# Kernel tuning notes

Measured on AMD Instinct MI355X. Metric: run time of the kernel, lower is better.

Reference implementation:

```python
import jax, jax.numpy as jnp
import numpy as np

N_EMBD = 512
N_HEAD = 8
EPS = 1e-5


def setup_inputs() -> dict:
    key = jax.random.key(0)
    ks = jax.random.split(key, 8)
    C = N_EMBD
    s = lambda k, shape, fan: jax.random.normal(k, shape, jnp.float32) * (1.0 / np.sqrt(fan))
    return {
        "x": jax.random.normal(ks[0], (2, 4096, C), jnp.float32),
        "w_qkv": s(ks[1], (C, 3 * C), C), "b_qkv": jnp.zeros((3 * C,), jnp.float32),
        "w_attn_proj": s(ks[2], (C, C), C), "b_attn_proj": jnp.zeros((C,), jnp.float32),
        "w_fc": s(ks[3], (C, 4 * C), C), "b_fc": jnp.zeros((4 * C,), jnp.float32),
        "w_mlp_proj": s(ks[4], (4 * C, C), 4 * C), "b_mlp_proj": jnp.zeros((C,), jnp.float32),
        "ln1_g": jnp.ones((C,), jnp.float32), "ln1_b": jnp.zeros((C,), jnp.float32),
        "ln2_g": jnp.ones((C,), jnp.float32), "ln2_b": jnp.zeros((C,), jnp.float32),
    }


def _layernorm(x, g, b):
    mu = jnp.mean(x, axis=-1, keepdims=True)
    var = jnp.mean(jnp.square(x - mu), axis=-1, keepdims=True)
    return (x - mu) * jax.lax.rsqrt(var + EPS) * g + b


def _attention(x, w_qkv, b_qkv, w_proj, b_proj):
    B, T, C = x.shape
    hd = C // N_HEAD
    qkv = x @ w_qkv + b_qkv  # [B,T,3C]
    q, k, v = jnp.split(qkv, 3, axis=-1)
    q = q.reshape(B, T, N_HEAD, hd)
    k = k.reshape(B, T, N_HEAD, hd)
    v = v.reshape(B, T, N_HEAD, hd)
    # NOTE: faithful to source -- scale by sqrt(C) (n_embd), not sqrt(head_dim)
    scores = jnp.einsum('bthd,bshd->bhts', q, k) / jnp.sqrt(jnp.float32(C))
    mask = jnp.tril(jnp.ones((T, T), bool))
    scores = jnp.where(mask, scores, -jnp.inf)
    attn = jax.nn.softmax(scores, axis=-1)  # [B,H,T,T]
    y = jnp.einsum('bhts,bshd->bthd', attn, v).reshape(B, T, C)
    return y @ w_proj + b_proj


def _mlp(x, w_fc, b_fc, w_proj, b_proj):
    h = jax.nn.gelu(x @ w_fc + b_fc, approximate=True)
    return h @ w_proj + b_proj


def reference(x, w_qkv, b_qkv, w_attn_proj, b_attn_proj, w_fc, b_fc,
              w_mlp_proj, b_mlp_proj, ln1_g, ln1_b, ln2_g, ln2_b):
    x = x + _attention(_layernorm(x, ln1_g, ln1_b), w_qkv, b_qkv, w_attn_proj, b_attn_proj)
    x = x + _mlp(_layernorm(x, ln2_g, ln2_b), w_fc, b_fc, w_mlp_proj, b_mlp_proj)
    return x
```

## Files before the change

### kernel.cpp

```cpp
#include <hip/hip_runtime.h>
#include <hip/hip_bf16.h>
#include <math.h>

constexpr int B_ = 2;
constexpr int T_ = 4096;
constexpr int C_ = 512;
constexpr int H_ = 8;
constexpr int BT_ = B_ * T_;
constexpr float EPS_ = 1e-5f;

typedef __attribute__((ext_vector_type(8))) short bf16x8;
typedef __attribute__((ext_vector_type(4))) short short4v;
typedef __attribute__((ext_vector_type(8))) short short8v;
typedef __attribute__((ext_vector_type(4))) float f32x4;

__device__ __forceinline__ short f2bf(float f) {
    unsigned int u = __float_as_uint(f);
    unsigned int r = (u + 0x7fffu + ((u >> 16) & 1u)) >> 16;
    return (short)r;
}
__device__ __forceinline__ float bf2f(short s) {
    return __uint_as_float(((unsigned)(unsigned short)s) << 16);
}
__device__ __forceinline__ short f2bf_h(float f) {
    union { __hip_bfloat16 h; short s; } u;
    u.h = __float2bfloat16(f);
    return u.s;
}
__device__ __forceinline__ float exp2_f(float x) {
    float r;
    asm("v_exp_f32 %0, %1" : "=v"(r) : "v"(x));
    return r;
}

__device__ __forceinline__ float gelu_f(float v) {
    const float k0 = 0.7978845608028654f;
    const float k1 = 0.044715f;
    return 0.5f * v * (1.0f + tanhf(k0 * (v + k1 * v * v * v)));
}

__device__ __forceinline__ void gl_lds16(const short* gsrc, short* lds) {
    __builtin_amdgcn_global_load_lds(
        (const __attribute__((address_space(1))) void*)gsrc,
        (__attribute__((address_space(3))) void*)lds, 16, 0, 0);
}

__global__ __launch_bounds__(256) void transpose_w4(
    const float* __restrict__ W0, short* __restrict__ D0,
    const float* __restrict__ W1, short* __restrict__ D1,
    const float* __restrict__ W2, short* __restrict__ D2,
    const float* __restrict__ W3, short* __restrict__ D3) {
    __shared__ float tile[32][33];
    int bid = blockIdx.x;
    const float* W; short* D; int K, N, nx;
    if (bid < 768)       {             W = W0; D = D0; K = 512;  N = 1536; nx = 48; }
    else if (bid < 1024) { bid -= 768;  W = W1; D = D1; K = 512;  N = 512;  nx = 16; }
    else if (bid < 2048) { bid -= 1024; W = W2; D = D2; K = 512;  N = 2048; nx = 64; }
    else                 { bid -= 2048; W = W3; D = D3; K = 2048; N = 512;  nx = 16; }
    const int n0 = (bid % nx) * 32, k0 = (bid / nx) * 32;
    const int tx = threadIdx.x & 31, ty = threadIdx.x >> 5;
    #pragma unroll
    for (int j = 0; j < 4; j++)
        tile[ty + j * 8][tx] = W[(size_t)(k0 + ty + j * 8) * N + n0 + tx];
    __syncthreads();
    #pragma unroll
    for (int j = 0; j < 4; j++)
        D[(size_t)(n0 + ty + j * 8) * K + k0 + tx] = f2bf(tile[tx][ty + j * 8]);
}

__global__ __launch_bounds__(256) void ln_bf16(const float* __restrict__ x,
                                               const float* __restrict__ g,
                                               const float* __restrict__ b,
                                               short* __restrict__ out) {
    const int row = blockIdx.x * 4 + (threadIdx.x >> 6);
    const int lane = threadIdx.x & 63;
    const float* xr = x + (size_t)row * C_;

    float4 v0 = *(const float4*)(xr + lane * 8);
    float4 v1 = *(const float4*)(xr + lane * 8 + 4);

    float s  = v0.x + v0.y + v0.z + v0.w + v1.x + v1.y + v1.z + v1.w;
    float s2 = v0.x*v0.x + v0.y*v0.y + v0.z*v0.z + v0.w*v0.w
             + v1.x*v1.x + v1.y*v1.y + v1.z*v1.z + v1.w*v1.w;
    #pragma unroll
    for (int off = 32; off; off >>= 1) {
        s  += __shfl_down(s, off);
        s2 += __shfl_down(s2, off);
    }
    s  = __shfl(s, 0);
    s2 = __shfl(s2, 0);

    const float mu  = s * (1.0f / C_);
    const float var = s2 * (1.0f / C_) - mu * mu;
    const float rs  = rsqrtf(var + EPS_);

    float4 g0 = *(const float4*)(g + lane * 8);
    float4 g1 = *(const float4*)(g + lane * 8 + 4);
    float4 b0 = *(const float4*)(b + lane * 8);
    float4 b1 = *(const float4*)(b + lane * 8 + 4);

    short8v o;
    o[0] = f2bf((v0.x - mu) * rs * g0.x + b0.x);
    o[1] = f2bf((v0.y - mu) * rs * g0.y + b0.y);
    o[2] = f2bf((v0.z - mu) * rs * g0.z + b0.z);
    o[3] = f2bf((v0.w - mu) * rs * g0.w + b0.w);
    o[4] = f2bf((v1.x - mu) * rs * g1.x + b1.x);
    o[5] = f2bf((v1.y - mu) * rs * g1.y + b1.y);
    o[6] = f2bf((v1.z - mu) * rs * g1.z + b1.z);
    o[7] = f2bf((v1.w - mu) * rs * g1.w + b1.w);
    *(short8v*)(out + (size_t)row * C_ + lane * 8) = o;
}

template<int ACT, int OUTBF16, int HASRES, int VFUSE>
__global__ __launch_bounds__(256) void gemm_bf16(const short* __restrict__ A,
                                                 const short* __restrict__ Wt,
                                                 const float* __restrict__ bias,
                                                 const float* __restrict__ res,
                                                 void* __restrict__ outp,
                                                 int M, int N, int K,
                                                 int GX, int CY,
                                                 short* __restrict__ vtb) {
    __shared__ short As[64 * 128];
    __shared__ short Bs[128 * 128];

    const int bid = blockIdx.x;
    const int xcd = bid & 7, jb = bid >> 3;
    const int by = xcd * CY + jb / GX;
    const int bx = jb % GX;

    const int t = threadIdx.x;
    const int w = t >> 6;
    const int l = t & 63;
    const int c = l & 15;
    const int g = l >> 4;
    const int wr = w >> 1, wc = w & 1;
    const int m0 = by * 64, n0 = bx * 128;

    const int r16 = t >> 4;
    const int sch = ((t & 15) ^ (r16 & 7)) * 8;
    const short* Asrc = A  + (size_t)(m0 + r16) * K + sch;
    const short* Bsrc = Wt + (size_t)(n0 + r16) * K + sch;

    auto stage = [&](int kt) {
        #pragma unroll
        for (int i = 0; i < 4; i++)
            gl_lds16(Asrc + (size_t)(16 * i) * K + kt, &As[i * 2048 + w * 512]);
        #pragma unroll
        for (int i = 0; i < 8; i++)
            gl_lds16(Bsrc + (size_t)(16 * i) * K + kt, &Bs[i * 2048 + w * 512]);
    };

    f32x4 acc[2][4] = {};

    for (int kt = 0; kt < K; kt += 128) {
        stage(kt);
        __syncthreads();

        #pragma unroll
        for (int j = 0; j < 4; j++) {
            const int ckj = ((4 * j + g) ^ (c & 7)) * 8;
            bf16x8 af[2], bfr[4];
            #pragma unroll
            for (int mt = 0; mt < 2; mt++)
                af[mt] = *(const bf16x8*)&As[(wr * 32 + mt * 16 + c) * 128 + ckj];
            #pragma unroll
            for (int nt = 0; nt < 4; nt++)
                bfr[nt] = *(const bf16x8*)&Bs[(wc * 64 + nt * 16 + c) * 128 + ckj];
            #pragma unroll
            for (int mt = 0; mt < 2; mt++)
                #pragma unroll
                for (int nt = 0; nt < 4; nt++)
                    acc[mt][nt] = __builtin_amdgcn_mfma_f32_16x16x32_bf16(
                        af[mt], bfr[nt], acc[mt][nt], 0, 0, 0);
        }

        __syncthreads();
    }

    const int colb = n0 + wc * 64;
    float bias_v[4];
    #pragma unroll
    for (int nt = 0; nt < 4; nt++) bias_v[nt] = bias[colb + nt * 16 + c];

    if (VFUSE && n0 >= 1024) {
        const int bq   = m0 >> 12;
        const int trow = (m0 & 4095) + wr * 32;
        #pragma unroll
        for (int mt = 0; mt < 2; mt++) {
            const int tb = trow + 8 * g + 4 * mt;
            #pragma unroll
            for (int nt = 0; nt < 4; nt++) {
                const int vcol = colb + nt * 16 + c - 1024;
                const int hh = vcol >> 6, dd = vcol & 63;
                short4v pk;
                #pragma unroll
                for (int rr = 0; rr < 4; rr++)
                    pk[rr] = f2bf(acc[mt][nt][rr] + bias_v[nt]);
                *(short4v*)&vtb[((size_t)((bq * 8 + hh) * 64 + dd)) * T_ + tb] = pk;
            }
        }
        return;
    }

    float* out_f = (float*)outp;
    short* out_h = (short*)outp;

    #pragma unroll
    for (int mt = 0; mt < 2; mt++) {
        #pragma unroll
        for (int rr = 0; rr < 4; rr++) {
            const size_t row = (size_t)(m0 + wr * 32 + mt * 16 + 4 * g + rr);
            #pragma unroll
            for (int nt = 0; nt < 4; nt++) {
                const int col = colb + nt * 16 + c;
                float v = acc[mt][nt][rr] + bias_v[nt];
                if (ACT) v = gelu_f(v);
                if (HASRES) v += res[row * N + col];
                if (OUTBF16) out_h[row * N + col] = f2bf(v);
                else         out_f[row * N + col] = v;
            }
        }
    }
}

__global__ __launch_bounds__(256) void attn_mfma(const short* __restrict__ qkv,
                                                 const short* __restrict__ Vt,
                                                 short* __restrict__ y) {
    __shared__ union {
        struct { short K[2][64 * 64]; short V[2][64 * 64]; } s;
        float O[4][16][68];
    } sm;

    const int bid = blockIdx.x;
    const int xcd = bid & 7, jj = bid >> 3;
    const int lo = jj >> 6;
    const int qtr = jj & 63;
    const int qt = (qtr < 32) ? (63 - qtr) : (qtr - 32);
    const int g16 = xcd * 2 + lo;
    const int b = g16 >> 3, h = g16 & 7;

    const int tid = threadIdx.x, w = tid >> 6, lid = tid & 63;
    const int c = lid & 15, g = lid >> 4;
    const size_t base = (size_t)b * T_;
    const int bh = g16;

    const float qmul = 0.04419417382415922f * 1.4426950408889634f;

    bf16x8 qf0, qf1;
    {
        const short* qa = qkv + (base + qt * 64 + w * 16 + c) * 1536 + h * 64 + g * 8;
        bf16x8 a0 = *(const bf16x8*)qa;
        bf16x8 a1 = *(const bf16x8*)(qa + 32);
        #pragma unroll
        for (int i = 0; i < 8; i++) {
            qf0[i] = f2bf_h(bf2f(a0[i]) * qmul);
            qf1[i] = f2bf_h(bf2f(a1[i]) * qmul);
        }
    }

    const f32x4 kZero = {0.f, 0.f, 0.f, 0.f};
    bf16x8 kOnes;
    #pragma unroll
    for (int i = 0; i < 8; i++) kOnes[i] = (short)0x3F80;

    f32x4 ot[4] = {};
    f32x4 lacc = {0.f, 0.f, 0.f, 0.f};
    const int qg = qt * 64 + w * 16 + c;

    const int sr = tid >> 3;
    const int sc = ((tid & 7) ^ (sr & 7)) * 8;

    auto stage = [&](short* Kb, short* Vb, int st) {
        const short* ks = qkv + (base + st * 64 + sr) * 1536 + 512 + h * 64 + sc;
        const short* vs = Vt + ((size_t)(bh * 64 + sr)) * T_ + st * 64 + sc;
        gl_lds16(ks, Kb + w * 512);
        gl_lds16(ks + (size_t)32 * 1536, Kb + 2048 + w * 512);
        gl_lds16(vs, Vb + w * 512);
        gl_lds16(vs + (size_t)32 * T_, Vb + 2048 + w * 512);
    };

    const int rx = c & 7;
    const int ck0 = g ^ rx;
    const int ck1 = ck0 ^ 4;

    auto tile = [&](const short* Kb, const short* Vb, bool mask_diag) {
        f32x4 s[4];
        __builtin_amdgcn_s_setprio(1);
        #pragma unroll
        for (int mt = 0; mt < 4; mt++) {
            const short* krow = Kb + (mt * 16 + c) * 64;
            bf16x8 k0 = *(const bf16x8*)&krow[ck0 * 8];
            bf16x8 k1 = *(const bf16x8*)&krow[ck1 * 8];
            f32x4 z = __builtin_amdgcn_mfma_f32_16x16x32_bf16(k0, qf0, kZero, 0, 0, 0);
            s[mt] = __builtin_amdgcn_mfma_f32_16x16x32_bf16(k1, qf1, z, 0, 0, 0);
        }
        __builtin_amdgcn_s_setprio(0);

        float p[4][4];
        #pragma unroll
        for (int mt = 0; mt < 4; mt++)
            #pragma unroll
            for (int rr = 0; rr < 4; rr++) {
                float v = s[mt][rr];
                if (mask_diag && (qt * 64 + mt * 16 + 4 * g + rr > qg)) v = -1e30f;
                p[mt][rr] = exp2_f(v);
            }

        bf16x8 pb0, pb1;
        #pragma unroll
        for (int i = 0; i < 8; i++) {
            pb0[i] = f2bf_h(p[(i >> 2)][i & 3]);
            pb1[i] = f2bf_h(p[2 + (i >> 2)][i & 3]);
        }
        __builtin_amdgcn_s_setprio(1);
        lacc = __builtin_amdgcn_mfma_f32_16x16x32_bf16(kOnes, pb0, lacc, 0, 0, 0);
        lacc = __builtin_amdgcn_mfma_f32_16x16x32_bf16(kOnes, pb1, lacc, 0, 0, 0);
        #pragma unroll
        for (int dt = 0; dt < 4; dt++) {
            const short* vrow = Vb + (16 * dt + c) * 64;
            bf16x8 va0 = *(const bf16x8*)&vrow[ck0 * 8];
            bf16x8 va1 = *(const bf16x8*)&vrow[ck1 * 8];
            ot[dt] = __builtin_amdgcn_mfma_f32_16x16x32_bf16(va0, pb0, ot[dt], 0, 0, 0);
            ot[dt] = __builtin_amdgcn_mfma_f32_16x16x32_bf16(va1, pb1, ot[dt], 0, 0, 0);
        }
        __builtin_amdgcn_s_setprio(0);
    };

    short* K0 = sm.s.K[0]; short* K1 = sm.s.K[1];
    short* V0 = sm.s.V[0]; short* V1 = sm.s.V[1];

    stage(K0, V0, 0);
    asm volatile("s_waitcnt vmcnt(0)" ::: "memory");
    __syncthreads();

    int st = 0;
    while (st + 2 <= qt) {
        stage(K1, V1, st + 1);
        tile(K0, V0, false);
        asm volatile("s_waitcnt vmcnt(0)" ::: "memory");
        __syncthreads();
        stage(K0, V0, st + 2);
        tile(K1, V1, false);
        asm volatile("s_waitcnt vmcnt(0)" ::: "memory");
        __syncthreads();
        st += 2;
    }
    if (st < qt) {
        stage(K1, V1, st + 1);
        tile(K0, V0, false);
        asm volatile("s_waitcnt vmcnt(0)" ::: "memory");
        __syncthreads();
        tile(K1, V1, true);
    } else {
        tile(K0, V0, true);
    }
    __syncthreads();

    const float inv = 1.0f / lacc[0];
    #pragma unroll
    for (int dt = 0; dt < 4; dt++)
        #pragma unroll
        for (int rr = 0; rr < 4; rr++)
            sm.O[w][c][16 * dt + 4 * g + rr] = ot[dt][rr] * inv;
    const int q = lid >> 2, ch = lid & 3;
    short* dst = y + (base + qt * 64 + w * 16 + q) * 512 + h * 64 + ch * 16;
    short8v o0, o1;
    #pragma unroll
    for (int j = 0; j < 8; j++) o0[j] = f2bf(sm.O[w][q][ch * 16 + j]);
    #pragma unroll
    for (int j = 0; j < 8; j++) o1[j] = f2bf(sm.O[w][q][ch * 16 + 8 + j]);
    *(short8v*)dst = o0;
    *(short8v*)(dst + 8) = o1;
}

extern "C" void kernel_launch(void* const* d_in, const int* in_sizes, int n_in,
                              void* d_out, int out_size, void* d_ws, size_t ws_size,
                              hipStream_t stream) {
    const float* x           = (const float*)d_in[0];
    const float* w_qkv       = (const float*)d_in[1];
    const float* b_qkv       = (const float*)d_in[2];
    const float* w_attn_proj = (const float*)d_in[3];
    const float* b_attn_proj = (const float*)d_in[4];
    const float* w_fc        = (const float*)d_in[5];
    const float* b_fc        = (const float*)d_in[6];
    const float* w_mlp_proj  = (const float*)d_in[7];
    const float* b_mlp_proj  = (const float*)d_in[8];
    const float* ln1_g       = (const float*)d_in[9];
    const float* ln1_b       = (const float*)d_in[10];
    const float* ln2_g       = (const float*)d_in[11];
    const float* ln2_b       = (const float*)d_in[12];

    float* out = (float*)d_out;
    short* ws16 = (short*)d_ws;

    short* wqkvT = ws16;
    short* waT   = wqkvT + 1536 * 512;
    short* wfcT  = waT   + 512 * 512;
    short* wmT   = wfcT  + 2048 * 512;
    short* xn    = wmT   + 512 * 2048;
    short* ybuf  = xn    + (size_t)BT_ * 512;
    short* qkvh  = ybuf  + (size_t)BT_ * 512;
    short* vtb   = qkvh  + (size_t)BT_ * 2048;

    transpose_w4<<<3072, 256, 0, stream>>>(w_qkv, wqkvT, w_attn_proj, waT,
                                           w_fc, wfcT, w_mlp_proj, wmT);

    ln_bf16<<<BT_ / 4, 256, 0, stream>>>(x, ln1_g, ln1_b, xn);

    gemm_bf16<0, 1, 0, 1><<<12 * 128, 256, 0, stream>>>(
        xn, wqkvT, b_qkv, nullptr, qkvh, BT_, 1536, 512, 12, 16, vtb);

    attn_mfma<<<1024, 256, 0, stream>>>(qkvh, vtb, ybuf);

    gemm_bf16<0, 0, 1, 0><<<4 * 128, 256, 0, stream>>>(
        ybuf, waT, b_attn_proj, x, out, BT_, 512, 512, 4, 16, nullptr);

    ln_bf16<<<BT_ / 4, 256, 0, stream>>>(out, ln2_g, ln2_b, xn);

    gemm_bf16<1, 1, 0, 0><<<16 * 128, 256, 0, stream>>>(
        xn, wfcT, b_fc, nullptr, qkvh, BT_, 2048, 512, 16, 16, nullptr);

    gemm_bf16<0, 0, 1, 0><<<4 * 128, 256, 0, stream>>>(
        qkvh, wmT, b_mlp_proj, out, out, BT_, 512, 2048, 4, 16, nullptr);
}
```

Baseline: 173.5 us.

## Process 128 queries per attention block with 8 waves sharing K/V tiles

The attention kernel now launches 512 blocks of 512 threads. Each block covers a 128-row query tile with eight waves, so every K/V tile staged into LDS is reused by twice as many query rows, which halves global K/V traffic per query. Each thread now stages one chunk of K and one of V per tile, and the loop runs to 2*Qt+2 tiles with per-wave causal skipping and diagonal masking. Blocks are paired across the two heads on each XCD in opposite causal order to balance load. The cost is that the first four waves sit idle on the last tile and larger blocks may lower occupancy.

```diff
diff --git a/kernel.cpp b/kernel.cpp
--- a/kernel.cpp
+++ b/kernel.cpp
@@ -223,19 +223,19 @@
     }
 }
 
-__global__ __launch_bounds__(256) void attn_mfma(const short* __restrict__ qkv,
+__global__ __launch_bounds__(512) void attn_mfma(const short* __restrict__ qkv,
                                                  const short* __restrict__ Vt,
                                                  short* __restrict__ y) {
     __shared__ union {
         struct { short K[2][64 * 64]; short V[2][64 * 64]; } s;
-        float O[4][16][68];
+        float O[8][16][68];
     } sm;
 
     const int bid = blockIdx.x;
     const int xcd = bid & 7, jj = bid >> 3;
-    const int lo = jj >> 6;
-    const int qtr = jj & 63;
-    const int qt = (qtr < 32) ? (63 - qtr) : (qtr - 32);
+    const int lo = jj >> 5;
+    const int qtr = jj & 31;
+    const int Qt = lo ? (31 - qtr) : qtr;
     const int g16 = xcd * 2 + lo;
     const int b = g16 >> 3, h = g16 & 7;
 
@@ -248,7 +248,7 @@
 
     bf16x8 qf0, qf1;
     {
-        const short* qa = qkv + (base + qt * 64 + w * 16 + c) * 1536 + h * 64 + g * 8;
+        const short* qa = qkv + (base + Qt * 128 + w * 16 + c) * 1536 + h * 64 + g * 8;
         bf16x8 a0 = *(const bf16x8*)qa;
         bf16x8 a1 = *(const bf16x8*)(qa + 32);
         #pragma unroll
@@ -265,7 +265,9 @@
 
     f32x4 ot[4] = {};
     f32x4 lacc = {0.f, 0.f, 0.f, 0.f};
-    const int qg = qt * 64 + w * 16 + c;
+    const int qg = Qt * 128 + w * 16 + c;
+    const int dw = 2 * Qt + (w >> 2);
+    const int NT = 2 * Qt + 2;
 
     const int sr = tid >> 3;
     const int sc = ((tid & 7) ^ (sr & 7)) * 8;
@@ -274,9 +276,7 @@
         const short* ks = qkv + (base + st * 64 + sr) * 1536 + 512 + h * 64 + sc;
         const short* vs = Vt + ((size_t)(bh * 64 + sr)) * T_ + st * 64 + sc;
         gl_lds16(ks, Kb + w * 512);
-        gl_lds16(ks + (size_t)32 * 1536, Kb + 2048 + w * 512);
         gl_lds16(vs, Vb + w * 512);
-        gl_lds16(vs + (size_t)32 * T_, Vb + 2048 + w * 512);
     };
 
     const int rx = c & 7;
@@ -302,7 +302,7 @@
             #pragma unroll
             for (int rr = 0; rr < 4; rr++) {
                 float v = s[mt][rr];
-                if (mask_diag && (qt * 64 + mt * 16 + 4 * g + rr > qg)) v = -1e30f;
+                if (mask_diag && (dw * 64 + mt * 16 + 4 * g + rr > qg)) v = -1e30f;
                 p[mt][rr] = exp2_f(v);
             }
 
@@ -334,27 +334,17 @@
     __syncthreads();
 
     int st = 0;
-    while (st + 2 <= qt) {
-        stage(K1, V1, st + 1);
-        tile(K0, V0, false);
+    while (st + 2 <= NT) {
+        if (st + 1 < NT) stage(K1, V1, st + 1);
+        if (st <= dw) tile(K0, V0, st == dw);
         asm volatile("s_waitcnt vmcnt(0)" ::: "memory");
         __syncthreads();
-        stage(K0, V0, st + 2);
-        tile(K1, V1, false);
+        if (st + 2 < NT) stage(K0, V0, st + 2);
+        if (st + 1 <= dw) tile(K1, V1, st + 1 == dw);
         asm volatile("s_waitcnt vmcnt(0)" ::: "memory");
         __syncthreads();
         st += 2;
     }
-    if (st < qt) {
-        stage(K1, V1, st + 1);
-        tile(K0, V0, false);
-        asm volatile("s_waitcnt vmcnt(0)" ::: "memory");
-        __syncthreads();
-        tile(K1, V1, true);
-    } else {
-        tile(K0, V0, true);
-    }
-    __syncthreads();
 
     const float inv = 1.0f / lacc[0];
     #pragma unroll
@@ -363,7 +353,7 @@
         for (int rr = 0; rr < 4; rr++)
             sm.O[w][c][16 * dt + 4 * g + rr] = ot[dt][rr] * inv;
     const int q = lid >> 2, ch = lid & 3;
-    short* dst = y + (base + qt * 64 + w * 16 + q) * 512 + h * 64 + ch * 16;
+    short* dst = y + (base + Qt * 128 + w * 16 + q) * 512 + h * 64 + ch * 16;
     short8v o0, o1;
     #pragma unroll
     for (int j = 0; j < 8; j++) o0[j] = f2bf(sm.O[w][q][ch * 16 + j]);
@@ -410,7 +400,7 @@
     gemm_bf16<0, 1, 0, 1><<<12 * 128, 256, 0, stream>>>(
         xn, wqkvT, b_qkv, nullptr, qkvh, BT_, 1536, 512, 12, 16, vtb);
 
-    attn_mfma<<<1024, 256, 0, stream>>>(qkvh, vtb, ybuf);
+    attn_mfma<<<512, 512, 0, stream>>>(qkvh, vtb, ybuf);
 
     gemm_bf16<0, 0, 1, 0><<<4 * 128, 256, 0, stream>>>(
         ybuf, waT, b_attn_proj, x, out, BT_, 512, 512, 4, 16, nullptr);
```

After: 170.3 us. No clear change (-1.8%).
